# Optimization experiments

Measured on AMD Instinct MI355X. Metric: run time of the kernel, lower is better.

The kernel has to match this reference:

```python
import jax, jax.numpy as jnp
import numpy as np

C = 512          # in_channels
N1 = 8192        # level-1 nodes
N2 = 131072      # level-2 nodes
N = 1 + N1 + N2  # total nodes (node 0 = root)
E = 1_000_000    # edges
STEP = 10        # ceil(1/ratio), ratio=0.1
K1 = (N1 + STEP - 1) // STEP   # 820 level-1 clusters
K2 = 4 * K1                    # max level-2 clusters (4 centers per parent)
M = 1 + K1 + K2                # coarse node count


def setup_inputs() -> dict:
    key = jax.random.key(0)
    ks = jax.random.split(key, 6)
    x = jax.random.normal(ks[0], (N, C), dtype=jnp.float32)
    edge_index = jax.random.randint(ks[1], (2, E), 0, N, dtype=jnp.int32)
    # fixed hierarchy layout: node 0 root, nodes 1..N1 level-1, rest level-2
    node_type = jnp.concatenate([jnp.zeros(1, jnp.int32),
                                 jnp.ones(N1, jnp.int32),
                                 jnp.full((N2,), 2, jnp.int32)])
    # tree: level-2 nodes point to a level-1 parent (global idx in [1, N1])
    tree = jax.random.randint(ks[2], (N,), 1, N1 + 1, dtype=jnp.int32)
    x_y_index = jax.random.uniform(ks[3], (N, 2), dtype=jnp.float32) * 100.0
    weight_1 = jax.random.normal(ks[4], (1, C), dtype=jnp.float32) * 0.04
    weight_2 = jax.random.normal(ks[5], (1, C), dtype=jnp.float32) * 0.04
    return {"x": x, "edge_index": edge_index, "node_type": node_type,
            "tree": tree, "x_y_index": x_y_index,
            "weight_1": weight_1, "weight_2": weight_2}


def _pair_dist(a, b):
    # a:[m,3], b:[n,3]; xy euclidean distance + |fitness diff| (euclidean_dist)
    dxy = jnp.sqrt(jnp.sum((a[:, None, :2] - b[None, :, :2]) ** 2, axis=-1))
    df = jnp.abs(a[:, None, 2] - b[None, :, 2])
    return dxy + df


def reference(x, edge_index, node_type, tree, x_y_index, weight_1, weight_2):
    x1, x2 = x[1:1 + N1], x[1 + N1:]
    xy1, xy2 = x_y_index[1:1 + N1], x_y_index[1 + N1:]

    # ---- level-1: fitness, threshold selection, cluster by nearest center ----
    f1 = jnp.tanh(jnp.sum(x1 * weight_1, axis=-1) / jnp.linalg.norm(weight_1))
    xyf1 = jnp.concatenate([xy1, f1[:, None]], axis=-1)          # [N1,3]
    order1 = jnp.argsort(f1)
    thr1 = order1[::STEP]                                        # [K1]
    d1 = _pair_dist(xyf1[thr1], xyf1)                            # [K1,N1]
    cluster_1 = jnp.argmin(d1, axis=0).astype(jnp.int32)         # [N1]

    # ---- level-2: fitness, 4 centers per parent cluster, nearest-center ----
    f2 = jnp.tanh(jnp.sum(x2 * weight_2, axis=-1) / jnp.linalg.norm(weight_2))
    xyf2 = jnp.concatenate([xy2, f2[:, None]], axis=-1)          # [N2,3]
    tree2 = tree[1 + N1:]
    parents = cluster_1[tree2 - jnp.min(tree2)]                  # [N2] in [0,K1)
    # pick 4 lowest-fitness members of each parent cluster as centers
    # (static-shape deterministic variant of random.sample over sorted fitness)
    comp_key = parents.astype(jnp.float32) * 4.0 + f2            # fitness in (-1,1)
    order2 = jnp.argsort(comp_key)
    p_sorted = parents[order2]
    counts = jax.ops.segment_sum(jnp.ones((N2,), jnp.int32), parents, K1)
    starts = jnp.concatenate([jnp.zeros(1, jnp.int32), jnp.cumsum(counts)[:-1]])
    rank = jnp.arange(N2, dtype=jnp.int32) - starts[p_sorted]
    row = jnp.where(rank < 4, p_sorted, K1)                      # overflow -> dummy row
    cand = jnp.full((K1 + 1, 4), -1, jnp.int32)
    cand = cand.at[row, jnp.clip(rank, 0, 3)].set(order2.astype(jnp.int32))[:K1]
    valid = cand >= 0                                            # [K1,4]
    cand_xyf = xyf2[jnp.where(valid, cand, 0)]                   # [K1,4,3]
    a = cand_xyf[parents]                                        # [N2,4,3]
    d2 = (jnp.sqrt(jnp.sum((a[..., :2] - xy2[:, None, :]) ** 2, axis=-1))
          + jnp.abs(a[..., 2] - f2[:, None]))
    d2 = jnp.where(valid[parents], d2, jnp.inf)
    local = jnp.argmin(d2, axis=1).astype(jnp.int32)             # [N2] in [0,4)
    cluster_2 = parents * 4 + local                              # [N2]

    # ---- merge cluster ids: [root | level-1 clusters | level-2 clusters] ----
    cluster = jnp.concatenate([jnp.zeros(1, jnp.int32),
                               cluster_1 + 1,
                               cluster_2 + 1 + K1])              # [N] in [0,M)

    # ---- scatter-mean pooling of features and coordinates ----
    cnt = jnp.maximum(jax.ops.segment_sum(jnp.ones((N, 1), x.dtype), cluster, M), 1.0)
    x_pool = jax.ops.segment_sum(x, cluster, M) / cnt            # [M,C]
    new_xy = jax.ops.segment_sum(x_y_index, cluster, M) / cnt    # [M,2]

    # ---- coarsen adjacency (self loops added on fine graph first) ----
    rows = jnp.concatenate([edge_index[0], jnp.arange(N, dtype=jnp.int32)])
    cols = jnp.concatenate([edge_index[1], jnp.arange(N, dtype=jnp.int32)])
    A = jnp.zeros((M, M), x.dtype).at[cluster[rows], cluster[cols]].add(1.0)

    new_node_type = jnp.concatenate([jnp.zeros(1, jnp.int32),
                                     jnp.ones(K1, jnp.int32),
                                     jnp.full((K2,), 2, jnp.int32)])
    new_tree = jnp.concatenate([jnp.full((1,), -1, jnp.int32),
                                jnp.zeros(K1, jnp.int32),
                                jnp.repeat(jnp.arange(1, K1 + 1, dtype=jnp.int32), 4)])
    fitness = jnp.concatenate([jnp.zeros(1, x.dtype), f1, f2])
    batch = jnp.zeros((M,), jnp.int32)
    return x_pool, A, batch, cluster, new_node_type, new_tree, fitness, new_xy
```

## Files before the change

### kernel.cpp

```cpp
#include <hip/hip_runtime.h>
#include <cstdint>
#include <cstddef>
#include <math.h>

#define C_     512
#define N1_    8192
#define N2_    131072
#define NTOT   139265
#define E_     1000000
#define K1_    820
#define K2_    3280
#define M_     4101
#define NB2    256
#define NBM    273

#define OFF_XPOOL   0ull
#define OFF_A       2099712ull
#define OFF_BATCH   18917913ull
#define OFF_CLUSTER 18922014ull
#define OFF_NNT     19061279ull
#define OFF_NTREE   19065380ull
#define OFF_FIT     19069481ull
#define OFF_NXY     19208746ull
#define OUT_TOTAL   19216948ull


__global__ void k_zero4(float4* __restrict__ p, long n4, float* __restrict__ tail, int ntail,
                        float* __restrict__ out) {
    long i = (long)blockIdx.x * blockDim.x + threadIdx.x;
    long stride = (long)gridDim.x * blockDim.x;
    float4 z = make_float4(0.f, 0.f, 0.f, 0.f);
    for (long k = i; k < n4; k += stride) p[k] = z;
    if (blockIdx.x == 0 && threadIdx.x < ntail) tail[threadIdx.x] = 0.f;
    if (i < M_) {
        out[OFF_NNT + i] = (i == 0) ? 0.0f : (i <= K1_ ? 1.0f : 2.0f);
        out[OFF_NTREE + i] = (i == 0) ? -1.0f : (i <= K1_ ? 0.0f : (float)(1 + (i - 1 - K1_) / 4));
        out[OFF_BATCH + i] = 0.0f;
        if (i == 0) out[OFF_FIT] = 0.0f;
    }
}

__device__ __forceinline__ float pairwise_combine(float r) {
    float o;
    o = __shfl_xor(r, 1, 64);  r = __fadd_rn(r, o);
    o = __shfl_xor(r, 2, 64);  r = __fadd_rn(r, o);
    o = __shfl_xor(r, 4, 64);  r = __fadd_rn(r, o);
    o = __shfl_xor(r, 8, 64);  r = __fadd_rn(r, o);
    o = __shfl_xor(r, 16, 64); r = __fadd_rn(r, o);
    return r;
}

__global__ void k_fit(const float* __restrict__ x, const float* __restrict__ w,
                      int rowOff, float* __restrict__ fs, float* __restrict__ fitOut) {
    __shared__ float wbuf[C_];
    __shared__ float xbuf[8][C_];
    for (int j = threadIdx.x; j < C_; j += 256) wbuf[j] = w[j];
    int wv = threadIdx.x >> 6, lane = threadIdx.x & 63;
    int rowA = blockIdx.x * 8 + wv * 2;
    const float4* rA = (const float4*)(x + (size_t)(rowOff + rowA) * C_);
    const float4* rB = (const float4*)(x + (size_t)(rowOff + rowA + 1) * C_);
    float4* xa = (float4*)xbuf[wv * 2];
    float4* xb = (float4*)xbuf[wv * 2 + 1];
    xa[lane] = rA[lane];
    xa[lane + 64] = rA[lane + 64];
    xb[lane] = rB[lane];
    xb[lane + 64] = rB[lane + 64];
    __syncthreads();
    int hl = lane & 31;
    int base = (hl >> 3) * 128 + (hl & 7);
    const float* xr = xbuf[wv * 2 + (lane >> 5)];
    float nv = wbuf[base];
    float nr = __fmul_rn(nv, nv);
    float r = __fmul_rn(xr[base], wbuf[base]);
    #pragma unroll
    for (int i = 1; i < 16; ++i) {
        int c = base + 8 * i;
        float u = wbuf[c];
        nr = __fadd_rn(nr, __fmul_rn(u, u));
        r = __fadd_rn(r, __fmul_rn(xr[c], u));
    }
    nr = pairwise_combine(nr);
    r = pairwise_combine(r);
    if (hl == 0) {
        float nrm = __fsqrt_rn(nr);
        float q = __fdiv_rn(r, nrm);
        float f = (float)tanh((double)q);
        int gw = rowA + (lane >> 5);
        fs[gw] = f;
        fitOut[gw] = f;
    }
}

#define RJ 512
__global__ void k_rank_partial(const float* __restrict__ f1s, int* __restrict__ rank) {
    __shared__ float buf[RJ];
    int i = blockIdx.x * 256 + threadIdx.x;
    int jbase = blockIdx.y * RJ;
    for (int j = threadIdx.x; j < RJ; j += 256) buf[j] = f1s[jbase + j];
    float fi = f1s[i];
    __syncthreads();
    int r = 0;
    #pragma unroll 8
    for (int j = 0; j < RJ; ++j) {
        float fj = buf[j];
        int jj = jbase + j;
        r += (int)((fj < fi) || (fj == fi && jj < i));
    }
    atomicAdd(&rank[i], r);
}

__global__ void k_thr(const int* __restrict__ rank, const float* __restrict__ xy,
                      const float* __restrict__ f1s, float* __restrict__ thrXYF) {
    int i = blockIdx.x * blockDim.x + threadIdx.x;
    if (i >= N1_) return;
    int r = rank[i];
    if (r % 10 == 0) {
        int k = r / 10;
        thrXYF[3 * k + 0] = xy[(size_t)(1 + i) * 2 + 0];
        thrXYF[3 * k + 1] = xy[(size_t)(1 + i) * 2 + 1];
        thrXYF[3 * k + 2] = f1s[i];
    }
}

__device__ __forceinline__ float pair_dist_f32(float ax, float ay, float af,
                                               float bx, float by, float bf) {
    float dx = __fsub_rn(ax, bx);
    float dy = __fsub_rn(ay, by);
    float dx2 = __fmul_rn(dx, dx);
    float dy2 = __fmul_rn(dy, dy);
    float ss = __fadd_rn(dx2, dy2);
    float dxy = __fsqrt_rn(ss);
    float df = fabsf(__fsub_rn(af, bf));
    return __fadd_rn(dxy, df);
}

__global__ void k_cluster1(const float* __restrict__ xy, const float* __restrict__ f1s,
                           const float* __restrict__ thrXYF,
                           int* __restrict__ cluster1, int* __restrict__ clusterAll,
                           float* __restrict__ outCluster, int* __restrict__ cntM) {
    __shared__ float t[K1_ * 3];
    for (int j = threadIdx.x; j < K1_ * 3; j += blockDim.x) t[j] = thrXYF[j];
    __syncthreads();
    if (blockIdx.x == 0 && threadIdx.x == 0) {
        clusterAll[0] = 0; outCluster[0] = 0.0f;
        atomicAdd(&cntM[0], 1);
    }
    int gw = blockIdx.x * (blockDim.x >> 6) + (threadIdx.x >> 6);
    int lane = threadIdx.x & 63;
    if (gw >= N1_) return;
    float xi = xy[(size_t)(1 + gw) * 2 + 0];
    float yi = xy[(size_t)(1 + gw) * 2 + 1];
    float fi = f1s[gw];
    float best = INFINITY; int bk = 0x7fffffff;
    for (int k = lane; k < K1_; k += 64) {
        float d = pair_dist_f32(t[3 * k + 0], t[3 * k + 1], t[3 * k + 2], xi, yi, fi);
        if (d < best || (d == best && k < bk)) { best = d; bk = k; }
    }
    for (int off = 32; off > 0; off >>= 1) {
        float ob = __shfl_down(best, off, 64);
        int ok = __shfl_down(bk, off, 64);
        if (ob < best || (ob == best && ok < bk)) { best = ob; bk = ok; }
    }
    if (lane == 0) {
        cluster1[gw] = bk;
        clusterAll[1 + gw] = bk + 1;
        outCluster[1 + gw] = (float)(bk + 1);
        atomicAdd(&cntM[bk + 1], 1);
    }
}

__global__ void k_mintree(const int* __restrict__ tree, int* __restrict__ minTree) {
    int i = blockIdx.x * blockDim.x + threadIdx.x;
    if (i >= N2_) return;
    int v = tree[1 + N1_ + i];
    for (int off = 32; off > 0; off >>= 1) v = min(v, __shfl_down(v, off, 64));
    if ((threadIdx.x & 63) == 0) atomicMin(minTree, v);
}

__global__ void k_parents(const int* __restrict__ tree, const int* __restrict__ cluster1,
                          const int* __restrict__ minTree,
                          int* __restrict__ parents, int* __restrict__ countP) {
    int i = blockIdx.x * blockDim.x + threadIdx.x;
    if (i >= N2_) return;
    int p = cluster1[tree[1 + N1_ + i] - minTree[0]];
    parents[i] = p;
    atomicAdd(&countP[p], 1);
}

__global__ void k_scan(const int* __restrict__ cnt, int* __restrict__ start, int n) {
    __shared__ int partial[1024];
    int t = threadIdx.x;
    int per = (n + 1023) / 1024;
    int lo = t * per;
    int hi = lo + per; if (hi > n) hi = n;
    int s = 0;
    if (lo < n) for (int i = lo; i < hi; ++i) s += cnt[i];
    partial[t] = s;
    __syncthreads();
    for (int off = 1; off < 1024; off <<= 1) {
        int v = (t >= off) ? partial[t - off] : 0;
        __syncthreads();
        partial[t] += v;
        __syncthreads();
    }
    int base = (t > 0) ? partial[t - 1] : 0;
    if (lo < n) for (int i = lo; i < hi; ++i) { start[i] = base; base += cnt[i]; }
    if (t == 1023) start[n] = partial[1023];
}

__global__ void kA_count(const int* __restrict__ parents, int* __restrict__ bc) {
    __shared__ int hist[K1_];
    for (int j = threadIdx.x; j < K1_; j += 512) hist[j] = 0;
    __syncthreads();
    int i = blockIdx.x * 512 + threadIdx.x;
    atomicAdd(&hist[parents[i]], 1);
    __syncthreads();
    for (int j = threadIdx.x; j < K1_; j += 512) bc[(size_t)j * NB2 + blockIdx.x] = hist[j];
}

__global__ void kA_scan(const int* __restrict__ startP, int* __restrict__ bc) {
    int p = blockIdx.x * 256 + threadIdx.x;
    if (p >= K1_) return;
    int run = startP[p];
    int* row = bc + (size_t)p * NB2;
    for (int b = 0; b < NB2; ++b) { int t = row[b]; row[b] = run; run += t; }
}

__global__ void kA_place(const int* __restrict__ parents, const int* __restrict__ bc,
                         int* __restrict__ plist) {
    __shared__ int par[512];
    int i = blockIdx.x * 512 + threadIdx.x;
    int p = parents[i];
    par[threadIdx.x] = p;
    __syncthreads();
    int rank = 0;
    for (int j = 0; j < (int)threadIdx.x; ++j) rank += (par[j] == p);
    plist[bc[(size_t)p * NB2 + blockIdx.x] + rank] = i;
}

__global__ void kM_count(const int* __restrict__ clusterAll, int* __restrict__ bc) {
    __shared__ int hist[M_];
    for (int j = threadIdx.x; j < M_; j += 512) hist[j] = 0;
    __syncthreads();
    int i = blockIdx.x * 512 + threadIdx.x;
    if (i < NTOT) atomicAdd(&hist[clusterAll[i]], 1);
    __syncthreads();
    for (int j = threadIdx.x; j < M_; j += 512) bc[(size_t)j * NBM + blockIdx.x] = hist[j];
}

__global__ void kM_scan(const int* __restrict__ startM, int* __restrict__ bc) {
    int c = blockIdx.x * 256 + threadIdx.x;
    if (c >= M_) return;
    int run = startM[c];
    int* row = bc + (size_t)c * NBM;
    for (int b = 0; b < NBM; ++b) { int t = row[b]; row[b] = run; run += t; }
}

__global__ void kM_place(const int* __restrict__ clusterAll, const int* __restrict__ bc,
                         int* __restrict__ lst) {
    __shared__ int par[512];
    int i = blockIdx.x * 512 + threadIdx.x;
    int c = (i < NTOT) ? clusterAll[i] : -1;
    par[threadIdx.x] = c;
    __syncthreads();
    if (i >= NTOT) return;
    int rank = 0;
    for (int j = 0; j < (int)threadIdx.x; ++j) rank += (par[j] == c);
    lst[bc[(size_t)c * NBM + blockIdx.x] + rank] = i;
}

__global__ void k_top4(const int* __restrict__ startP, const int* __restrict__ plist,
                       const float* __restrict__ f2s, int* __restrict__ cand) {
    int p = blockIdx.x * (blockDim.x >> 6) + (threadIdx.x >> 6);
    int lane = threadIdx.x & 63;
    if (p >= K1_) return;
    int lo = startP[p], hi = startP[p + 1];
    float base = (float)(4 * p);
    float bk[4] = {INFINITY, INFINITY, INFINITY, INFINITY};
    int bi[4] = {-1, -1, -1, -1};
    for (int q = lo + lane; q < hi; q += 64) {
        int idx = plist[q];
        float key = __fadd_rn(base, f2s[idx]);
        for (int j = 0; j < 4; ++j) {
            bool less = (key < bk[j]) || (key == bk[j] && (unsigned)idx < (unsigned)bi[j]);
            if (less) {
                for (int r = 3; r > j; --r) { bk[r] = bk[r - 1]; bi[r] = bi[r - 1]; }
                bk[j] = key; bi[j] = idx;
                break;
            }
        }
    }
    for (int off = 1; off < 64; off <<= 1) {
        float ok_[4]; int oi[4];
        for (int j = 0; j < 4; ++j) {
            ok_[j] = __shfl_xor(bk[j], off, 64);
            oi[j]  = __shfl_xor(bi[j], off, 64);
        }
        float nk[4]; int ni[4];
        int ia = 0, ib = 0;
        for (int j = 0; j < 4; ++j) {
            bool takeA = (bk[ia] < ok_[ib]) ||
                         (bk[ia] == ok_[ib] && (unsigned)bi[ia] <= (unsigned)oi[ib]);
            if (takeA) { nk[j] = bk[ia]; ni[j] = bi[ia]; ++ia; }
            else       { nk[j] = ok_[ib]; ni[j] = oi[ib]; ++ib; }
        }
        for (int j = 0; j < 4; ++j) { bk[j] = nk[j]; bi[j] = ni[j]; }
    }
    if (lane == 0) {
        for (int j = 0; j < 4; ++j) cand[4 * p + j] = bi[j];
    }
}

__global__ void k_cluster2(const float* __restrict__ xy, const float* __restrict__ f2s,
                           const int* __restrict__ parents, const int* __restrict__ cand,
                           int* __restrict__ clusterAll, float* __restrict__ outCluster,
                           int* __restrict__ cntM) {
    int i = blockIdx.x * blockDim.x + threadIdx.x;
    if (i >= N2_) return;
    int p = parents[i];
    float xi = xy[(size_t)(1 + N1_ + i) * 2 + 0];
    float yi = xy[(size_t)(1 + N1_ + i) * 2 + 1];
    float fi = f2s[i];
    float best = INFINITY; int bj = 0;
    for (int j = 0; j < 4; ++j) {
        int cidx = cand[4 * p + j];
        float d;
        if (cidx < 0) {
            d = INFINITY;
        } else {
            float ax = xy[(size_t)(1 + N1_ + cidx) * 2 + 0];
            float ay = xy[(size_t)(1 + N1_ + cidx) * 2 + 1];
            float af = f2s[cidx];
            d = pair_dist_f32(ax, ay, af, xi, yi, fi);
        }
        if (d < best) { best = d; bj = j; }
    }
    int c2 = p * 4 + bj;
    int c = c2 + 1 + K1_;
    clusterAll[1 + N1_ + i] = c;
    outCluster[1 + N1_ + i] = (float)c;
    atomicAdd(&cntM[c], 1);
}

__global__ void k_pool(const float* __restrict__ x, const float* __restrict__ xy,
                       const int* __restrict__ startM, const int* __restrict__ clusterList,
                       float* __restrict__ out) {
    int m = blockIdx.x;
    int lo = startM[m], hi = startM[m + 1];
    int t = threadIdx.x;
    double s0 = 0.0, s1 = 0.0, s2 = 0.0, s3 = 0.0, sx = 0.0, sy = 0.0;
    int q = lo;
    for (; q + 1 < hi; q += 2) {
        int n0 = clusterList[q];
        int n1 = clusterList[q + 1];
        float4 a = ((const float4*)(x + (size_t)n0 * C_))[t];
        float4 b = ((const float4*)(x + (size_t)n1 * C_))[t];
        s0 += (double)a.x; s1 += (double)a.y; s2 += (double)a.z; s3 += (double)a.w;
        s0 += (double)b.x; s1 += (double)b.y; s2 += (double)b.z; s3 += (double)b.w;
        if (t == 0) sx += (double)xy[(size_t)n0 * 2 + 0] + (double)xy[(size_t)n1 * 2 + 0];
        if (t == 1) sy += (double)xy[(size_t)n0 * 2 + 1] + (double)xy[(size_t)n1 * 2 + 1];
    }
    if (q < hi) {
        int n0 = clusterList[q];
        float4 a = ((const float4*)(x + (size_t)n0 * C_))[t];
        s0 += (double)a.x; s1 += (double)a.y; s2 += (double)a.z; s3 += (double)a.w;
        if (t == 0) sx += (double)xy[(size_t)n0 * 2 + 0];
        if (t == 1) sy += (double)xy[(size_t)n0 * 2 + 1];
    }
    double cnt = (double)((hi - lo) > 0 ? (hi - lo) : 1);
    float4* xp = (float4*)(out + OFF_XPOOL + (size_t)m * C_);
    xp[t] = make_float4((float)(s0 / cnt), (float)(s1 / cnt),
                        (float)(s2 / cnt), (float)(s3 / cnt));
    if (t == 0) out[OFF_NXY + 2 * (size_t)m + 0] = (float)(sx / cnt);
    if (t == 1) out[OFF_NXY + 2 * (size_t)m + 1] = (float)(sy / cnt);
}

__global__ void k_edges(const int* __restrict__ ei, const int* __restrict__ clusterAll,
                        float* __restrict__ A) {
    int i = blockIdx.x * blockDim.x + threadIdx.x;
    if (i < E_) {
        int r = clusterAll[ei[i]];
        int c = clusterAll[ei[E_ + i]];
        atomicAdd(&A[(size_t)r * M_ + c], 1.0f);
    } else {
        int n = i - E_;
        if (n < NTOT) {
            int c = clusterAll[n];
            atomicAdd(&A[(size_t)c * M_ + c], 1.0f);
        }
    }
}

extern "C" void kernel_launch(void* const* d_in, const int* in_sizes, int n_in,
                              void* d_out, int out_size, void* d_ws, size_t ws_size,
                              hipStream_t stream) {
    const float* x    = (const float*)d_in[0];
    const int*   ei   = (const int*)d_in[1];
    const int*   tree = (const int*)d_in[3];
    const float* xy   = (const float*)d_in[4];
    const float* w1   = (const float*)d_in[5];
    const float* w2   = (const float*)d_in[6];
    float* out = (float*)d_out;

    char* p = (char*)d_ws;
    auto alloc = [&](size_t nbytes) -> char* {
        char* r = p;
        p += (nbytes + 255) & ~(size_t)255;
        return r;
    };
    float*  f1s        = (float*)alloc((size_t)N1_ * 4);
    float*  f2s        = (float*)alloc((size_t)N2_ * 4);
    float*  thrXYF     = (float*)alloc((size_t)K1_ * 3 * 4);
    int*    cluster1   = (int*)alloc((size_t)N1_ * 4);
    int*    clusterAll = (int*)alloc((size_t)NTOT * 4);
    int*    parentsA   = (int*)alloc((size_t)N2_ * 4);
    int*    plist      = (int*)alloc((size_t)N2_ * 4);
    int*    clusterLst = (int*)alloc((size_t)NTOT * 4);
    int*    startP     = (int*)alloc((size_t)(K1_ + 1) * 4);
    int*    startM     = (int*)alloc((size_t)(M_ + 1) * 4);
    int*    bcP        = (int*)alloc((size_t)K1_ * NB2 * 4);
    int*    bcM        = (int*)alloc((size_t)M_ * NBM * 4);
    size_t zeroInts = (size_t)(K1_ + M_ + N1_);
    char*   zeroBlk    = alloc(zeroInts * 4);
    int*    countP     = (int*)zeroBlk;
    int*    cntM       = countP + K1_;
    int*    rankArr    = cntM + M_;
    int*    cand       = (int*)alloc((size_t)K1_ * 4 * 4);
    int*    minTree    = (int*)alloc(4);

    hipMemsetAsync(zeroBlk, 0, zeroInts * 4, stream);
    hipMemsetAsync(minTree, 0x7F, 4, stream);

    {
        long nA = (long)M_ * M_;
        long n4 = nA / 4;
        int ntail = (int)(nA - n4 * 4);
        float* A = out + OFF_A;
        k_zero4<<<4096, 256, 0, stream>>>((float4*)A, n4, A + n4 * 4, ntail, out);
    }

    k_fit<<<N1_ / 8, 256, 0, stream>>>(x, w1, 1, f1s, out + OFF_FIT + 1);
    k_fit<<<N2_ / 8, 256, 0, stream>>>(x, w2, 1 + N1_, f2s, out + OFF_FIT + 1 + N1_);
    {
        dim3 g(N1_ / 256, N1_ / RJ);
        k_rank_partial<<<g, 256, 0, stream>>>(f1s, rankArr);
    }
    k_thr<<<N1_ / 256, 256, 0, stream>>>(rankArr, xy, f1s, thrXYF);
    k_cluster1<<<N1_ / 4, 256, 0, stream>>>(xy, f1s, thrXYF, cluster1, clusterAll,
                                            out + OFF_CLUSTER, cntM);
    k_mintree<<<N2_ / 256, 256, 0, stream>>>(tree, minTree);
    k_parents<<<N2_ / 256, 256, 0, stream>>>(tree, cluster1, minTree, parentsA, countP);
    k_scan<<<1, 1024, 0, stream>>>(countP, startP, K1_);
    kA_count<<<NB2, 512, 0, stream>>>(parentsA, bcP);
    kA_scan<<<(K1_ + 255) / 256, 256, 0, stream>>>(startP, bcP);
    kA_place<<<NB2, 512, 0, stream>>>(parentsA, bcP, plist);
    k_top4<<<(K1_ + 3) / 4, 256, 0, stream>>>(startP, plist, f2s, cand);
    k_cluster2<<<N2_ / 256, 256, 0, stream>>>(xy, f2s, parentsA, cand, clusterAll,
                                              out + OFF_CLUSTER, cntM);
    k_scan<<<1, 1024, 0, stream>>>(cntM, startM, M_);
    kM_count<<<NBM, 512, 0, stream>>>(clusterAll, bcM);
    kM_scan<<<(M_ + 255) / 256, 256, 0, stream>>>(startM, bcM);
    kM_place<<<NBM, 512, 0, stream>>>(clusterAll, bcM, clusterLst);
    k_pool<<<M_, 128, 0, stream>>>(x, xy, startM, clusterLst, out);
    k_edges<<<(E_ + NTOT + 255) / 256, 256, 0, stream>>>(ei, clusterAll, out + OFF_A);
}
```

Before: 798.3 us.

## Fuse small launches and parallelize per-row block-offset scans with wave shuffles

Folds the min-tree reduction into the zeroing kernel, storing the negated value so an atomicMax against the zero-initialised buffer replaces the separate memset and kernel. The two single-block scans now run as an extra block inside the count kernels. The per-row block-offset scans move from one serial thread per row to one wavefront per row using shuffle prefix sums, and the pooling loop is unrolled by four to keep more loads in flight. The goal is fewer kernel launches and shorter serial scan chains, at the cost of more complex kernels; the scan blocks fused into the count kernels rely on their inputs being complete from earlier kernels, which still holds given the launch order.

```diff
diff --git a/kernel.cpp b/kernel.cpp
--- a/kernel.cpp
+++ b/kernel.cpp
@@ -26,7 +26,8 @@
 
 
 __global__ void k_zero4(float4* __restrict__ p, long n4, float* __restrict__ tail, int ntail,
-                        float* __restrict__ out) {
+                        float* __restrict__ out,
+                        const int* __restrict__ tree, int* __restrict__ minTreeNeg) {
     long i = (long)blockIdx.x * blockDim.x + threadIdx.x;
     long stride = (long)gridDim.x * blockDim.x;
     float4 z = make_float4(0.f, 0.f, 0.f, 0.f);
@@ -37,6 +38,12 @@
         out[OFF_NTREE + i] = (i == 0) ? -1.0f : (i <= K1_ ? 0.0f : (float)(1 + (i - 1 - K1_) / 4));
         out[OFF_BATCH + i] = 0.0f;
         if (i == 0) out[OFF_FIT] = 0.0f;
+    }
+    if (i < N2_) {
+        int v = tree[1 + N1_ + (int)i];
+        int u = 0x7FFFFFFF - v;
+        for (int off = 32; off > 0; off >>= 1) u = max(u, __shfl_down(u, off, 64));
+        if ((threadIdx.x & 63) == 0) atomicMax(minTreeNeg, u);
     }
 }
 
@@ -169,35 +176,29 @@
     }
 }
 
-__global__ void k_mintree(const int* __restrict__ tree, int* __restrict__ minTree) {
-    int i = blockIdx.x * blockDim.x + threadIdx.x;
-    if (i >= N2_) return;
-    int v = tree[1 + N1_ + i];
-    for (int off = 32; off > 0; off >>= 1) v = min(v, __shfl_down(v, off, 64));
-    if ((threadIdx.x & 63) == 0) atomicMin(minTree, v);
-}
-
 __global__ void k_parents(const int* __restrict__ tree, const int* __restrict__ cluster1,
-                          const int* __restrict__ minTree,
+                          const int* __restrict__ minTreeNeg,
                           int* __restrict__ parents, int* __restrict__ countP) {
     int i = blockIdx.x * blockDim.x + threadIdx.x;
     if (i >= N2_) return;
-    int p = cluster1[tree[1 + N1_ + i] - minTree[0]];
+    int mt = 0x7FFFFFFF - minTreeNeg[0];
+    int p = cluster1[tree[1 + N1_ + i] - mt];
     parents[i] = p;
     atomicAdd(&countP[p], 1);
 }
 
-__global__ void k_scan(const int* __restrict__ cnt, int* __restrict__ start, int n) {
-    __shared__ int partial[1024];
+__device__ __forceinline__ void scan_block512(const int* __restrict__ cnt,
+                                              int* __restrict__ start, int n) {
+    __shared__ int partial[512];
     int t = threadIdx.x;
-    int per = (n + 1023) / 1024;
+    int per = (n + 511) / 512;
     int lo = t * per;
     int hi = lo + per; if (hi > n) hi = n;
     int s = 0;
     if (lo < n) for (int i = lo; i < hi; ++i) s += cnt[i];
     partial[t] = s;
     __syncthreads();
-    for (int off = 1; off < 1024; off <<= 1) {
+    for (int off = 1; off < 512; off <<= 1) {
         int v = (t >= off) ? partial[t - off] : 0;
         __syncthreads();
         partial[t] += v;
@@ -205,10 +206,12 @@
     }
     int base = (t > 0) ? partial[t - 1] : 0;
     if (lo < n) for (int i = lo; i < hi; ++i) { start[i] = base; base += cnt[i]; }
-    if (t == 1023) start[n] = partial[1023];
-}
-
-__global__ void kA_count(const int* __restrict__ parents, int* __restrict__ bc) {
+    if (t == 511) start[n] = partial[511];
+}
+
+__global__ void kA_count_scanP(const int* __restrict__ parents, int* __restrict__ bc,
+                               const int* __restrict__ countP, int* __restrict__ startP) {
+    if (blockIdx.x == NB2) { scan_block512(countP, startP, K1_); return; }
     __shared__ int hist[K1_];
     for (int j = threadIdx.x; j < K1_; j += 512) hist[j] = 0;
     __syncthreads();
@@ -219,11 +222,24 @@
 }
 
 __global__ void kA_scan(const int* __restrict__ startP, int* __restrict__ bc) {
-    int p = blockIdx.x * 256 + threadIdx.x;
+    int wv = threadIdx.x >> 6, lane = threadIdx.x & 63;
+    int p = blockIdx.x * 4 + wv;
     if (p >= K1_) return;
-    int run = startP[p];
-    int* row = bc + (size_t)p * NB2;
-    for (int b = 0; b < NB2; ++b) { int t = row[b]; row[b] = run; run += t; }
+    int4* row = (int4*)(bc + (size_t)p * NB2);
+    int4 v = row[lane];
+    int s = v.x + v.y + v.z + v.w;
+    int xsc = s;
+    for (int off = 1; off < 64; off <<= 1) {
+        int y = __shfl_up(xsc, off, 64);
+        if (lane >= off) xsc += y;
+    }
+    int base = startP[p] + xsc - s;
+    int4 o;
+    o.x = base;
+    o.y = o.x + v.x;
+    o.z = o.y + v.y;
+    o.w = o.z + v.z;
+    row[lane] = o;
 }
 
 __global__ void kA_place(const int* __restrict__ parents, const int* __restrict__ bc,
@@ -238,7 +254,9 @@
     plist[bc[(size_t)p * NB2 + blockIdx.x] + rank] = i;
 }
 
-__global__ void kM_count(const int* __restrict__ clusterAll, int* __restrict__ bc) {
+__global__ void kM_count_scanM(const int* __restrict__ clusterAll, int* __restrict__ bc,
+                               const int* __restrict__ cntM, int* __restrict__ startM) {
+    if (blockIdx.x == NBM) { scan_block512(cntM, startM, M_); return; }
     __shared__ int hist[M_];
     for (int j = threadIdx.x; j < M_; j += 512) hist[j] = 0;
     __syncthreads();
@@ -249,11 +267,29 @@
 }
 
 __global__ void kM_scan(const int* __restrict__ startM, int* __restrict__ bc) {
-    int c = blockIdx.x * 256 + threadIdx.x;
+    int wv = threadIdx.x >> 6, lane = threadIdx.x & 63;
+    int c = blockIdx.x * 4 + wv;
     if (c >= M_) return;
-    int run = startM[c];
     int* row = bc + (size_t)c * NBM;
-    for (int b = 0; b < NBM; ++b) { int t = row[b]; row[b] = run; run += t; }
+    int t[5]; int s = 0;
+    int b0 = lane * 5;
+    #pragma unroll
+    for (int k = 0; k < 5; ++k) {
+        int b = b0 + k;
+        t[k] = (b < NBM) ? row[b] : 0;
+        s += t[k];
+    }
+    int xsc = s;
+    for (int off = 1; off < 64; off <<= 1) {
+        int y = __shfl_up(xsc, off, 64);
+        if (lane >= off) xsc += y;
+    }
+    int run = startM[c] + xsc - s;
+    #pragma unroll
+    for (int k = 0; k < 5; ++k) {
+        int b = b0 + k;
+        if (b < NBM) { row[b] = run; run += t[k]; }
+    }
 }
 
 __global__ void kM_place(const int* __restrict__ clusterAll, const int* __restrict__ bc,
@@ -350,6 +386,28 @@
     int t = threadIdx.x;
     double s0 = 0.0, s1 = 0.0, s2 = 0.0, s3 = 0.0, sx = 0.0, sy = 0.0;
     int q = lo;
+    for (; q + 3 < hi; q += 4) {
+        int n0 = clusterList[q];
+        int n1 = clusterList[q + 1];
+        int n2 = clusterList[q + 2];
+        int n3 = clusterList[q + 3];
+        float4 a = ((const float4*)(x + (size_t)n0 * C_))[t];
+        float4 b = ((const float4*)(x + (size_t)n1 * C_))[t];
+        float4 c = ((const float4*)(x + (size_t)n2 * C_))[t];
+        float4 d = ((const float4*)(x + (size_t)n3 * C_))[t];
+        s0 += (double)a.x; s1 += (double)a.y; s2 += (double)a.z; s3 += (double)a.w;
+        s0 += (double)b.x; s1 += (double)b.y; s2 += (double)b.z; s3 += (double)b.w;
+        s0 += (double)c.x; s1 += (double)c.y; s2 += (double)c.z; s3 += (double)c.w;
+        s0 += (double)d.x; s1 += (double)d.y; s2 += (double)d.z; s3 += (double)d.w;
+        if (t == 0) {
+            sx += (double)xy[(size_t)n0 * 2 + 0] + (double)xy[(size_t)n1 * 2 + 0];
+            sx += (double)xy[(size_t)n2 * 2 + 0] + (double)xy[(size_t)n3 * 2 + 0];
+        }
+        if (t == 1) {
+            sy += (double)xy[(size_t)n0 * 2 + 1] + (double)xy[(size_t)n1 * 2 + 1];
+            sy += (double)xy[(size_t)n2 * 2 + 1] + (double)xy[(size_t)n3 * 2 + 1];
+        }
+    }
     for (; q + 1 < hi; q += 2) {
         int n0 = clusterList[q];
         int n1 = clusterList[q + 1];
@@ -420,23 +478,23 @@
     int*    startM     = (int*)alloc((size_t)(M_ + 1) * 4);
     int*    bcP        = (int*)alloc((size_t)K1_ * NB2 * 4);
     int*    bcM        = (int*)alloc((size_t)M_ * NBM * 4);
-    size_t zeroInts = (size_t)(K1_ + M_ + N1_);
+    size_t zeroInts = (size_t)(K1_ + M_ + N1_ + 1);
     char*   zeroBlk    = alloc(zeroInts * 4);
     int*    countP     = (int*)zeroBlk;
     int*    cntM       = countP + K1_;
     int*    rankArr    = cntM + M_;
+    int*    minTreeNeg = rankArr + N1_;
     int*    cand       = (int*)alloc((size_t)K1_ * 4 * 4);
-    int*    minTree    = (int*)alloc(4);
 
     hipMemsetAsync(zeroBlk, 0, zeroInts * 4, stream);
-    hipMemsetAsync(minTree, 0x7F, 4, stream);
 
     {
         long nA = (long)M_ * M_;
         long n4 = nA / 4;
         int ntail = (int)(nA - n4 * 4);
         float* A = out + OFF_A;
-        k_zero4<<<4096, 256, 0, stream>>>((float4*)A, n4, A + n4 * 4, ntail, out);
+        k_zero4<<<4096, 256, 0, stream>>>((float4*)A, n4, A + n4 * 4, ntail, out,
+                                          tree, minTreeNeg);
     }
 
     k_fit<<<N1_ / 8, 256, 0, stream>>>(x, w1, 1, f1s, out + OFF_FIT + 1);
@@ -448,18 +506,15 @@
     k_thr<<<N1_ / 256, 256, 0, stream>>>(rankArr, xy, f1s, thrXYF);
     k_cluster1<<<N1_ / 4, 256, 0, stream>>>(xy, f1s, thrXYF, cluster1, clusterAll,
                                             out + OFF_CLUSTER, cntM);
-    k_mintree<<<N2_ / 256, 256, 0, stream>>>(tree, minTree);
-    k_parents<<<N2_ / 256, 256, 0, stream>>>(tree, cluster1, minTree, parentsA, countP);
-    k_scan<<<1, 1024, 0, stream>>>(countP, startP, K1_);
-    kA_count<<<NB2, 512, 0, stream>>>(parentsA, bcP);
-    kA_scan<<<(K1_ + 255) / 256, 256, 0, stream>>>(startP, bcP);
+    k_parents<<<N2_ / 256, 256, 0, stream>>>(tree, cluster1, minTreeNeg, parentsA, countP);
+    kA_count_scanP<<<NB2 + 1, 512, 0, stream>>>(parentsA, bcP, countP, startP);
+    kA_scan<<<(K1_ + 3) / 4, 256, 0, stream>>>(startP, bcP);
     kA_place<<<NB2, 512, 0, stream>>>(parentsA, bcP, plist);
     k_top4<<<(K1_ + 3) / 4, 256, 0, stream>>>(startP, plist, f2s, cand);
     k_cluster2<<<N2_ / 256, 256, 0, stream>>>(xy, f2s, parentsA, cand, clusterAll,
                                               out + OFF_CLUSTER, cntM);
-    k_scan<<<1, 1024, 0, stream>>>(cntM, startM, M_);
-    kM_count<<<NBM, 512, 0, stream>>>(clusterAll, bcM);
-    kM_scan<<<(M_ + 255) / 256, 256, 0, stream>>>(startM, bcM);
+    kM_count_scanM<<<NBM + 1, 512, 0, stream>>>(clusterAll, bcM, cntM, startM);
+    kM_scan<<<(M_ + 3) / 4, 256, 0, stream>>>(startM, bcM);
     kM_place<<<NBM, 512, 0, stream>>>(clusterAll, bcM, clusterLst);
     k_pool<<<M_, 128, 0, stream>>>(x, xy, startM, clusterLst, out);
     k_edges<<<(E_ + NTOT + 255) / 256, 256, 0, stream>>>(ei, clusterAll, out + OFF_A);
```

New measurement: 725.3 us. 9.2% less time.
